# Optimization experiments

Hardware: AMD Instinct MI355X
Metric: run time of the kernel (lower is better)

The kernel has to match this reference:

```python
import jax, jax.numpy as jnp
import numpy as np

D_EMB, N_HEADS = 1024, 16
D_K = D_EMB // N_HEADS

def setup_inputs() -> dict:
    key = jax.random.key(0)
    ks = jax.random.split(key, 5)
    scale = 0.02
    return {
        "n": jax.random.normal(ks[0], (2, 2048, D_EMB), dtype=jnp.float32),
        "W_q": jax.random.normal(ks[1], (D_EMB, D_EMB), dtype=jnp.float32) * scale,
        "W_k": jax.random.normal(ks[2], (D_EMB, D_EMB), dtype=jnp.float32) * scale,
        "W_v": jax.random.normal(ks[3], (D_EMB, D_EMB), dtype=jnp.float32) * scale,
        "W_o": jax.random.normal(ks[4], (D_EMB, D_EMB), dtype=jnp.float32) * scale,
    }

def reference(n, W_q, W_k, W_v, W_o):
    B, S, _ = n.shape
    # torch Linear(bias=False): y = x @ W.T, W is [out, in]
    def proj(x, W):
        y = jnp.einsum('bsd,ed->bse', x, W)
        return y.reshape(B, S, N_HEADS, D_K).transpose(0, 2, 1, 3)  # [B,H,S,Dk]
    Q, K, V = proj(n, W_q), proj(n, W_k), proj(n, W_v)
    A = jnp.einsum('bhqd,bhkd->bhqk', Q, K) * (D_K ** -0.5)
    A = jnp.clip(A, -5.0, 5.0)
    A = jax.nn.softmax(A, axis=-1)
    ctx = jnp.einsum('bhqk,bhkd->bhqd', A, V)  # [B,H,S,Dk]
    ctx = ctx.transpose(0, 2, 1, 3).reshape(B, S, D_EMB)
    return jnp.einsum('bsd,ed->bse', ctx, W_o)
```

## Files before the change

kernel.cpp:

```cpp
#include <hip/hip_runtime.h>
#include <hip/hip_bf16.h>
#include <stdint.h>

typedef __attribute__((ext_vector_type(4))) float floatx4;
typedef __attribute__((ext_vector_type(8))) short shortx8;
typedef __attribute__((ext_vector_type(4))) unsigned short ushortx4;
typedef __attribute__((ext_vector_type(8))) unsigned short ushortx8;
typedef __attribute__((ext_vector_type(2))) uint32_t uintx2;

#define MFMA16(a, b, c) __builtin_amdgcn_mfma_f32_16x16x32_bf16((a), (b), (c), 0, 0, 0)

__device__ inline unsigned short f2bf(float f) {
    union { float f; uint32_t u; } v; v.f = f;
    uint32_t u = v.u;
    return (unsigned short)((u + 0x7FFFu + ((u >> 16) & 1u)) >> 16);
}

#if defined(__has_builtin) && __has_builtin(__builtin_amdgcn_cvt_pk_bf16_f32)
__device__ inline uint32_t pkbf(float a, float b) {
    auto r = __builtin_amdgcn_cvt_pk_bf16_f32(a, b);
    union { decltype(r) v; uint32_t u; } x; x.v = r; return x.u;
}
#else
__device__ inline uint32_t pkbf(float a, float b) {
    return ((uint32_t)f2bf(b) << 16) | f2bf(a);
}
#endif

#if defined(__has_builtin) && __has_builtin(__builtin_amdgcn_exp2f)
#define EXP2F(x) __builtin_amdgcn_exp2f(x)
#else
#define EXP2F(x) __expf((x) * 0.69314718056f)
#endif

__device__ inline void gl2lds16(const void* g, void* l) {
    __builtin_amdgcn_global_load_lds(
        (const __attribute__((address_space(1))) void*)(uintptr_t)g,
        (__attribute__((address_space(3))) void*)(uintptr_t)l, 16, 0, 0);
}

__global__ void convert_all(const float* __restrict__ n, const float* __restrict__ wq,
                            const float* __restrict__ wk, const float* __restrict__ wv,
                            const float* __restrict__ wo,
                            unsigned short* __restrict__ nb, unsigned short* __restrict__ wqb,
                            unsigned short* __restrict__ wkb, unsigned short* __restrict__ wvb,
                            unsigned short* __restrict__ wob) {
    int i = blockIdx.x * 256 + threadIdx.x;
    const float* src; unsigned short* dst; int off;
    if (i < 1048576) { src = n; dst = nb; off = i; }
    else {
        int j = i - 1048576; int r = j >> 18; int o = j & 262143;
        src = (r == 0) ? wq : (r == 1) ? wk : (r == 2) ? wv : wo;
        dst = (r == 0) ? wqb : (r == 1) ? wkb : (r == 2) ? wvb : wob;
        off = o;
    }
    floatx4 f = ((const floatx4*)src)[off];
    uintx2 u;
    u.x = pkbf(f.x, f.y); u.y = pkbf(f.z, f.w);
    ((uintx2*)dst)[off] = u;
}

__device__ inline void gemm_tile_128(const unsigned short* __restrict__ A,
                                     const unsigned short* __restrict__ B,
                                     unsigned short* sA, unsigned short* sB,
                                     floatx4 acc[4][4]) {
    const int tid = threadIdx.x, w = tid >> 6, l = tid & 63;
    const int c = l & 15, quad = l >> 4;
    const int wm = (w >> 1) * 64, wn = (w & 1) * 64;
    for (int kt = 0; kt < 16; ++kt) {
        #pragma unroll
        for (int r = 0; r < 4; ++r) {
            int row = r * 32 + w * 8 + (l >> 3);
            int cb  = (l & 7) ^ (row & 7);
            gl2lds16(A + row * 1024 + kt * 64 + cb * 8, (char*)sA + r * 4096 + w * 1024 + l * 16);
            gl2lds16(B + row * 1024 + kt * 64 + cb * 8, (char*)sB + r * 4096 + w * 1024 + l * 16);
        }
        __syncthreads();
        #pragma unroll
        for (int ks = 0; ks < 2; ++ks) {
            shortx8 af[4], bfr[4];
            #pragma unroll
            for (int i2 = 0; i2 < 4; ++i2) {
                int ra = wm + i2 * 16 + c;
                af[i2] = *(const shortx8*)((const char*)sA + ra * 128 + (((ks * 4 + quad) ^ (ra & 7)) * 16));
                int rb = wn + i2 * 16 + c;
                bfr[i2] = *(const shortx8*)((const char*)sB + rb * 128 + (((ks * 4 + quad) ^ (rb & 7)) * 16));
            }
            #pragma unroll
            for (int i2 = 0; i2 < 4; ++i2)
                #pragma unroll
                for (int j2 = 0; j2 < 4; ++j2)
                    acc[i2][j2] = MFMA16(af[i2], bfr[j2], acc[i2][j2]);
        }
        __syncthreads();
    }
}

__global__ void gemm_qkv(const unsigned short* __restrict__ nb,
                         const unsigned short* __restrict__ wqb,
                         const unsigned short* __restrict__ wkb,
                         const unsigned short* __restrict__ wvb,
                         unsigned short* __restrict__ Qb, unsigned short* __restrict__ Kb,
                         unsigned short* __restrict__ VTg) {
    __shared__ unsigned short sAB[2 * 128 * 64];
    unsigned short* sA = sAB;
    unsigned short* sB = sAB + 128 * 64;
    const int mt = blockIdx.x, nt = blockIdx.y;
    const int region = nt >> 3, nl0 = (nt & 7) * 128;
    const unsigned short* W = (region == 0) ? wqb : (region == 1) ? wkb : wvb;
    floatx4 acc[4][4] = {};
    gemm_tile_128(nb + mt * 128 * 1024, W + nl0 * 1024, sA, sB, acc);
    const int tid = threadIdx.x, w = tid >> 6, l = tid & 63, c = l & 15, quad = l >> 4;
    const int wm = (w >> 1) * 64, wn = (w & 1) * 64;
    if (region < 2) {
        unsigned short* O = (region == 0) ? Qb : Kb;
        #pragma unroll
        for (int i2 = 0; i2 < 4; ++i2)
            #pragma unroll
            for (int j2 = 0; j2 < 4; ++j2)
                #pragma unroll
                for (int r = 0; r < 4; ++r) {
                    int row = wm + i2 * 16 + quad * 4 + r, col = wn + j2 * 16 + c;
                    sAB[row * 128 + col] = f2bf(acc[i2][j2][r]);
                }
        __syncthreads();
        #pragma unroll
        for (int t = 0; t < 8; ++t) {
            int off = t * 4096 + tid * 16;
            int row = off >> 8, colb = off & 255;
            *(ushortx8*)((char*)(O + (mt * 128 + row) * 1024 + nl0) + colb) =
                *(const ushortx8*)((const char*)sAB + off);
        }
    } else {
        const int hh = w & 1, tt = w >> 1;
        char* img = (char*)sAB + (hh * 2 + tt) * 8192;
        #pragma unroll
        for (int i2 = 0; i2 < 4; ++i2)
            #pragma unroll
            for (int j2 = 0; j2 < 4; ++j2) {
                int d = j2 * 16 + c;
                int blk = (i2 >> 1) * 4 + quad;
                int phys = blk ^ (d & 7);
                uintx2 v;
                v.x = pkbf(acc[i2][j2][0], acc[i2][j2][1]);
                v.y = pkbf(acc[i2][j2][2], acc[i2][j2][3]);
                *(uintx2*)(img + d * 128 + phys * 16 + (i2 & 1) * 8) = v;
            }
        __syncthreads();
        const int h0 = (nt & 7) * 2, t0 = mt * 2;
        #pragma unroll
        for (int g = 0; g < 8; ++g) {
            int off = g * 4096 + tid * 16;
            int hsel = off >> 14, within = off & 16383;
            *(ushortx8*)((char*)VTg + (h0 + hsel) * 524288 + t0 * 8192 + within) =
                *(const ushortx8*)((const char*)sAB + off);
        }
    }
}

__global__ void __launch_bounds__(256) gemm_out(const unsigned short* __restrict__ ctx,
                         const unsigned short* __restrict__ wob,
                         float* __restrict__ out) {
    __shared__ unsigned short sA[128 * 64];
    __shared__ unsigned short sB[64 * 64];
    __shared__ float sC[64 * 64];
    const int mt = blockIdx.x, nt = blockIdx.y;
    const unsigned short* A = ctx + mt * 128 * 1024;
    const unsigned short* B = wob + nt * 64 * 1024;
    const int tid = threadIdx.x, w = tid >> 6, l = tid & 63, c = l & 15, quad = l >> 4;
    const int srow = w * 8 + (l >> 3), scb = l & 7;
    floatx4 acc[2][4] = {};
    for (int kt = 0; kt < 16; ++kt) {
        #pragma unroll
        for (int r = 0; r < 4; ++r) {
            int row = r * 32 + srow, cb = scb ^ (row & 7);
            gl2lds16(A + row * 1024 + kt * 64 + cb * 8, (char*)sA + r * 4096 + w * 1024 + l * 16);
        }
        #pragma unroll
        for (int r = 0; r < 2; ++r) {
            int row = r * 32 + srow, cb = scb ^ (row & 7);
            gl2lds16(B + row * 1024 + kt * 64 + cb * 8, (char*)sB + r * 4096 + w * 1024 + l * 16);
        }
        __syncthreads();
        #pragma unroll
        for (int ks = 0; ks < 2; ++ks) {
            shortx8 af[2], bf2[4];
            #pragma unroll
            for (int i2 = 0; i2 < 2; ++i2) {
                int ra = w * 32 + i2 * 16 + c;
                af[i2] = *(const shortx8*)((const char*)sA + ra * 128 + (((ks * 4 + quad) ^ (ra & 7)) * 16));
            }
            #pragma unroll
            for (int j2 = 0; j2 < 4; ++j2) {
                int rb = j2 * 16 + c;
                bf2[j2] = *(const shortx8*)((const char*)sB + rb * 128 + (((ks * 4 + quad) ^ (rb & 7)) * 16));
            }
            #pragma unroll
            for (int i2 = 0; i2 < 2; ++i2)
                #pragma unroll
                for (int j2 = 0; j2 < 4; ++j2)
                    acc[i2][j2] = MFMA16(af[i2], bf2[j2], acc[i2][j2]);
        }
        __syncthreads();
    }
    #pragma unroll
    for (int half = 0; half < 2; ++half) {
        if ((w >> 1) == half) {
            #pragma unroll
            for (int i2 = 0; i2 < 2; ++i2)
                #pragma unroll
                for (int j2 = 0; j2 < 4; ++j2)
                    #pragma unroll
                    for (int r = 0; r < 4; ++r) {
                        int row = (w & 1) * 32 + i2 * 16 + quad * 4 + r, col = j2 * 16 + c;
                        sC[row * 64 + col] = acc[i2][j2][r];
                    }
        }
        __syncthreads();
        #pragma unroll
        for (int t = 0; t < 4; ++t) {
            int off = t * 4096 + tid * 16;
            int row = off >> 8, colb = off & 255;
            *(floatx4*)((char*)(out + (mt * 128 + half * 64 + row) * 1024 + nt * 64) + colb) =
                *(const floatx4*)((const char*)sC + off);
        }
        __syncthreads();
    }
}

__global__ void __launch_bounds__(256) attn(const unsigned short* __restrict__ Qb,
                     const unsigned short* __restrict__ Kb,
                     const unsigned short* __restrict__ VTg, unsigned short* __restrict__ ctx) {
    __shared__ unsigned short sQ[128 * 64];
    __shared__ unsigned short sK[2][64 * 64];
    __shared__ unsigned short sV[2][64 * 64];
    const int qt = blockIdx.x, h = blockIdx.y, b = blockIdx.z;
    const int tid = threadIdx.x, w = tid >> 6, l = tid & 63, c = l & 15, quad = l >> 4;
    const int tok0 = b * 2048 + qt * 128;
    const int srow = w * 8 + (l >> 3), scb = l & 7;
    #pragma unroll
    for (int r = 0; r < 4; ++r) {
        int row = r * 32 + srow, cb = scb ^ (row & 7);
        gl2lds16(Qb + (tok0 + row) * 1024 + h * 64 + cb * 8, (char*)sQ + r * 4096 + w * 1024 + l * 16);
    }
    const unsigned short* Kbase = Kb + b * 2048 * 1024 + h * 64;
    const char* Vbase = (const char*)VTg + h * 524288 + (size_t)b * 32 * 8192;
    #pragma unroll
    for (int r = 0; r < 2; ++r) {
        int row = r * 32 + srow, cb = scb ^ (row & 7);
        gl2lds16(Kbase + row * 1024 + cb * 8, (char*)sK[0] + r * 4096 + w * 1024 + l * 16);
        gl2lds16(Vbase + r * 4096 + w * 1024 + l * 16, (char*)sV[0] + r * 4096 + w * 1024 + l * 16);
    }
    __syncthreads();
    shortx8 qf[2][2];
    #pragma unroll
    for (int ks = 0; ks < 2; ++ks)
        #pragma unroll
        for (int qb = 0; qb < 2; ++qb) {
            int rq = w * 32 + qb * 16 + c;
            qf[ks][qb] = *(const shortx8*)((const char*)sQ + rq * 128 + (((ks * 4 + quad) ^ (rq & 7)) * 16));
        }
    floatx4 cacc[4][2] = {};
    float lacc[2] = {0.f, 0.f};
    const float SC = 0.18033688f;
    const float CLIP = 7.2134752f;
    for (int kt = 0; kt < 32; ++kt) {
        const int cur = kt & 1;
        if (kt < 31) {
            #pragma unroll
            for (int r = 0; r < 2; ++r) {
                int row = r * 32 + srow, cb = scb ^ (row & 7);
                gl2lds16(Kbase + ((kt + 1) * 64 + row) * 1024 + cb * 8,
                         (char*)sK[cur ^ 1] + r * 4096 + w * 1024 + l * 16);
                gl2lds16(Vbase + (kt + 1) * 8192 + r * 4096 + w * 1024 + l * 16,
                         (char*)sV[cur ^ 1] + r * 4096 + w * 1024 + l * 16);
            }
        }
        const unsigned short* sKc = sK[cur];
        const unsigned short* sVc = sV[cur];
        floatx4 s[2][4] = {};
        #pragma unroll
        for (int ks = 0; ks < 2; ++ks) {
            shortx8 ak[4];
            #pragma unroll
            for (int j = 0; j < 4; ++j) {
                int rk = j * 16 + c;
                ak[j] = *(const shortx8*)((const char*)sKc + rk * 128 + (((ks * 4 + quad) ^ (rk & 7)) * 16));
            }
            #pragma unroll
            for (int j = 0; j < 4; ++j)
                #pragma unroll
                for (int qb = 0; qb < 2; ++qb)
                    s[qb][j] = MFMA16(ak[j], qf[ks][qb], s[qb][j]);
        }
        #pragma unroll
        for (int qb = 0; qb < 2; ++qb) {
            float rs = 0.f;
            #pragma unroll
            for (int j = 0; j < 4; ++j)
                #pragma unroll
                for (int r = 0; r < 4; ++r) {
                    float v = s[qb][j][r] * SC;
                    v = fminf(fmaxf(v, -CLIP), CLIP);
                    v = EXP2F(v);
                    s[qb][j][r] = v;
                    rs += v;
                }
            rs += __shfl_xor(rs, 16);
            rs += __shfl_xor(rs, 32);
            lacc[qb] += rs;
        }
        #pragma unroll
        for (int chunk = 0; chunk < 2; ++chunk) {
            shortx8 av[4];
            #pragma unroll
            for (int di = 0; di < 4; ++di) {
                int rv = di * 16 + c;
                av[di] = *(const shortx8*)((const char*)sVc + rv * 128 + (((chunk * 4 + quad) ^ (rv & 7)) * 16));
            }
            shortx8 p[2];
            #pragma unroll
            for (int qb = 0; qb < 2; ++qb) {
                union { shortx8 v; uint32_t u[4]; } pk;
                pk.u[0] = pkbf(s[qb][2 * chunk][0], s[qb][2 * chunk][1]);
                pk.u[1] = pkbf(s[qb][2 * chunk][2], s[qb][2 * chunk][3]);
                pk.u[2] = pkbf(s[qb][2 * chunk + 1][0], s[qb][2 * chunk + 1][1]);
                pk.u[3] = pkbf(s[qb][2 * chunk + 1][2], s[qb][2 * chunk + 1][3]);
                p[qb] = pk.v;
            }
            #pragma unroll
            for (int di = 0; di < 4; ++di)
                #pragma unroll
                for (int qb = 0; qb < 2; ++qb)
                    cacc[di][qb] = MFMA16(av[di], p[qb], cacc[di][qb]);
        }
        if (kt < 31) __syncthreads();
    }
    #pragma unroll
    for (int qb = 0; qb < 2; ++qb) {
        float inv = 1.0f / lacc[qb];
        int row = tok0 + w * 32 + qb * 16 + c;
        #pragma unroll
        for (int di = 0; di < 4; ++di) {
            uintx2 v;
            v.x = pkbf(cacc[di][qb][0] * inv, cacc[di][qb][1] * inv);
            v.y = pkbf(cacc[di][qb][2] * inv, cacc[di][qb][3] * inv);
            *(uintx2*)(ctx + row * 1024 + h * 64 + di * 16 + quad * 4) = v;
        }
    }
}

extern "C" void kernel_launch(void* const* d_in, const int* in_sizes, int n_in,
                              void* d_out, int out_size, void* d_ws, size_t ws_size,
                              hipStream_t stream) {
    const float* n  = (const float*)d_in[0];
    const float* wq = (const float*)d_in[1];
    const float* wk = (const float*)d_in[2];
    const float* wv = (const float*)d_in[3];
    const float* wo = (const float*)d_in[4];
    float* out = (float*)d_out;
    char* ws = (char*)d_ws;
    unsigned short* nb  = (unsigned short*)(ws);
    unsigned short* wqb = (unsigned short*)(ws + 8388608);
    unsigned short* wkb = (unsigned short*)(ws + 10485760);
    unsigned short* wvb = (unsigned short*)(ws + 12582912);
    unsigned short* wob = (unsigned short*)(ws + 14680064);
    unsigned short* Qb  = (unsigned short*)(ws + 16777216);
    unsigned short* Kb  = (unsigned short*)(ws + 25165824);
    unsigned short* VTg = (unsigned short*)(ws + 33554432);
    unsigned short* ctx = (unsigned short*)(ws + 41943040);

    convert_all<<<dim3(8192), dim3(256), 0, stream>>>(n, wq, wk, wv, wo, nb, wqb, wkb, wvb, wob);
    gemm_qkv<<<dim3(32, 24), dim3(256), 0, stream>>>(nb, wqb, wkb, wvb, Qb, Kb, VTg);
    attn<<<dim3(16, 16, 2), dim3(256), 0, stream>>>(Qb, Kb, VTg, ctx);
    gemm_out<<<dim3(32, 16), dim3(256), 0, stream>>>(ctx, wob, out);
}
```

Measured before the change: 190.6 us.

## Process two KV tiles per attention iteration with quad-buffered LDS

```diff
diff --git a/kernel.cpp b/kernel.cpp
--- a/kernel.cpp
+++ b/kernel.cpp
@@ -31,6 +31,12 @@
 #define EXP2F(x) __builtin_amdgcn_exp2f(x)
 #else
 #define EXP2F(x) __expf((x) * 0.69314718056f)
+#endif
+
+#if defined(__has_builtin) && __has_builtin(__builtin_amdgcn_fmed3f)
+#define CLAMP3(x, lo, hi) __builtin_amdgcn_fmed3f((x), (lo), (hi))
+#else
+#define CLAMP3(x, lo, hi) fminf(fmaxf((x), (lo)), (hi))
 #endif
 
 __device__ inline void gl2lds16(const void* g, void* l) {
@@ -228,113 +234,89 @@
     }
 }
 
-__global__ void __launch_bounds__(256) attn(const unsigned short* __restrict__ Qb,
+__global__ void __launch_bounds__(256, 2) attn(const unsigned short* __restrict__ Qb,
                      const unsigned short* __restrict__ Kb,
                      const unsigned short* __restrict__ VTg, unsigned short* __restrict__ ctx) {
-    __shared__ unsigned short sQ[128 * 64];
-    __shared__ unsigned short sK[2][64 * 64];
-    __shared__ unsigned short sV[2][64 * 64];
+    __shared__ char lds[81920];
     const int qt = blockIdx.x, h = blockIdx.y, b = blockIdx.z;
     const int tid = threadIdx.x, w = tid >> 6, l = tid & 63, c = l & 15, quad = l >> 4;
     const int tok0 = b * 2048 + qt * 128;
-    const int srow = w * 8 + (l >> 3), scb = l & 7;
+    const int srow = w * 8 + (l >> 3);
+    const int cb = (l & 7) ^ (srow & 7);
     #pragma unroll
-    for (int r = 0; r < 4; ++r) {
-        int row = r * 32 + srow, cb = scb ^ (row & 7);
-        gl2lds16(Qb + (tok0 + row) * 1024 + h * 64 + cb * 8, (char*)sQ + r * 4096 + w * 1024 + l * 16);
-    }
+    for (int r = 0; r < 4; ++r)
+        gl2lds16(Qb + (tok0 + r * 32 + srow) * 1024 + h * 64 + cb * 8, lds + r * 4096 + w * 1024 + l * 16);
     const unsigned short* Kbase = Kb + b * 2048 * 1024 + h * 64;
-    const char* Vbase = (const char*)VTg + h * 524288 + (size_t)b * 32 * 8192;
-    #pragma unroll
-    for (int r = 0; r < 2; ++r) {
-        int row = r * 32 + srow, cb = scb ^ (row & 7);
-        gl2lds16(Kbase + row * 1024 + cb * 8, (char*)sK[0] + r * 4096 + w * 1024 + l * 16);
-        gl2lds16(Vbase + r * 4096 + w * 1024 + l * 16, (char*)sV[0] + r * 4096 + w * 1024 + l * 16);
-    }
+    const char* Vbase = (const char*)VTg + h * 524288 + (size_t)b * 262144;
+    const char* Ksrc = (const char*)(Kbase + srow * 1024 + cb * 8);
+    #define STAGE_K(kt, t) { _Pragma("unroll") for (int r = 0; r < 2; ++r) \
+        gl2lds16(Ksrc + (size_t)(kt) * 131072 + r * 65536, lds + 16384 + (t) * 8192 + r * 4096 + w * 1024 + l * 16); }
+    #define STAGE_V(kt, t) { _Pragma("unroll") for (int r = 0; r < 2; ++r) \
+        gl2lds16(Vbase + (kt) * 8192 + r * 4096 + w * 1024 + l * 16, lds + 49152 + (t) * 8192 + r * 4096 + w * 1024 + l * 16); }
+    STAGE_K(0, 0) STAGE_V(0, 0) STAGE_K(1, 1) STAGE_V(1, 1)
     __syncthreads();
+    int lb[2];
+    lb[0] = c * 128 + ((quad ^ (c & 7)) * 16);
+    lb[1] = c * 128 + (((4 + quad) ^ (c & 7)) * 16);
     shortx8 qf[2][2];
     #pragma unroll
     for (int ks = 0; ks < 2; ++ks)
         #pragma unroll
-        for (int qb = 0; qb < 2; ++qb) {
-            int rq = w * 32 + qb * 16 + c;
-            qf[ks][qb] = *(const shortx8*)((const char*)sQ + rq * 128 + (((ks * 4 + quad) ^ (rq & 7)) * 16));
-        }
+        for (int qb = 0; qb < 2; ++qb)
+            qf[ks][qb] = *(const shortx8*)(lds + (w * 2 + qb) * 2048 + lb[ks]);
     floatx4 cacc[4][2] = {};
     float lacc[2] = {0.f, 0.f};
     const float SC = 0.18033688f;
     const float CLIP = 7.2134752f;
-    for (int kt = 0; kt < 32; ++kt) {
-        const int cur = kt & 1;
-        if (kt < 31) {
-            #pragma unroll
-            for (int r = 0; r < 2; ++r) {
-                int row = r * 32 + srow, cb = scb ^ (row & 7);
-                gl2lds16(Kbase + ((kt + 1) * 64 + row) * 1024 + cb * 8,
-                         (char*)sK[cur ^ 1] + r * 4096 + w * 1024 + l * 16);
-                gl2lds16(Vbase + (kt + 1) * 8192 + r * 4096 + w * 1024 + l * 16,
-                         (char*)sV[cur ^ 1] + r * 4096 + w * 1024 + l * 16);
-            }
-        }
-        const unsigned short* sKc = sK[cur];
-        const unsigned short* sVc = sV[cur];
-        floatx4 s[2][4] = {};
-        #pragma unroll
-        for (int ks = 0; ks < 2; ++ks) {
-            shortx8 ak[4];
-            #pragma unroll
-            for (int j = 0; j < 4; ++j) {
-                int rk = j * 16 + c;
-                ak[j] = *(const shortx8*)((const char*)sKc + rk * 128 + (((ks * 4 + quad) ^ (rk & 7)) * 16));
-            }
-            #pragma unroll
-            for (int j = 0; j < 4; ++j)
-                #pragma unroll
-                for (int qb = 0; qb < 2; ++qb)
-                    s[qb][j] = MFMA16(ak[j], qf[ks][qb], s[qb][j]);
-        }
-        #pragma unroll
-        for (int qb = 0; qb < 2; ++qb) {
-            float rs = 0.f;
-            #pragma unroll
-            for (int j = 0; j < 4; ++j)
-                #pragma unroll
-                for (int r = 0; r < 4; ++r) {
-                    float v = s[qb][j][r] * SC;
-                    v = fminf(fmaxf(v, -CLIP), CLIP);
-                    v = EXP2F(v);
-                    s[qb][j][r] = v;
-                    rs += v;
-                }
-            rs += __shfl_xor(rs, 16);
-            rs += __shfl_xor(rs, 32);
-            lacc[qb] += rs;
-        }
-        #pragma unroll
-        for (int chunk = 0; chunk < 2; ++chunk) {
-            shortx8 av[4];
-            #pragma unroll
-            for (int di = 0; di < 4; ++di) {
-                int rv = di * 16 + c;
-                av[di] = *(const shortx8*)((const char*)sVc + rv * 128 + (((chunk * 4 + quad) ^ (rv & 7)) * 16));
-            }
-            shortx8 p[2];
-            #pragma unroll
-            for (int qb = 0; qb < 2; ++qb) {
-                union { shortx8 v; uint32_t u[4]; } pk;
-                pk.u[0] = pkbf(s[qb][2 * chunk][0], s[qb][2 * chunk][1]);
-                pk.u[1] = pkbf(s[qb][2 * chunk][2], s[qb][2 * chunk][3]);
-                pk.u[2] = pkbf(s[qb][2 * chunk + 1][0], s[qb][2 * chunk + 1][1]);
-                pk.u[3] = pkbf(s[qb][2 * chunk + 1][2], s[qb][2 * chunk + 1][3]);
-                p[qb] = pk.v;
-            }
-            #pragma unroll
-            for (int di = 0; di < 4; ++di)
-                #pragma unroll
-                for (int qb = 0; qb < 2; ++qb)
-                    cacc[di][qb] = MFMA16(av[di], p[qb], cacc[di][qb]);
-        }
-        if (kt < 31) __syncthreads();
+
+    #define COMPUTE_S(t, s) { _Pragma("unroll") for (int ks = 0; ks < 2; ++ks) { \
+        shortx8 ak[4]; \
+        _Pragma("unroll") for (int j = 0; j < 4; ++j) \
+            ak[j] = *(const shortx8*)(lds + 16384 + (t) * 8192 + j * 2048 + lb[ks]); \
+        _Pragma("unroll") for (int j = 0; j < 4; ++j) \
+            _Pragma("unroll") for (int qb = 0; qb < 2; ++qb) \
+                s[qb][j] = MFMA16(ak[j], qf[ks][qb], s[qb][j]); } }
+
+    #define SOFTMAX_T(s) { _Pragma("unroll") for (int qb = 0; qb < 2; ++qb) { \
+        float rs = 0.f; \
+        _Pragma("unroll") for (int j = 0; j < 4; ++j) \
+            _Pragma("unroll") for (int r = 0; r < 4; ++r) { \
+                float v = EXP2F(CLAMP3(s[qb][j][r] * SC, -CLIP, CLIP)); \
+                s[qb][j][r] = v; rs += v; } \
+        rs += __shfl_xor(rs, 16); rs += __shfl_xor(rs, 32); \
+        lacc[qb] += rs; } }
+
+    #define PV_T(t, s) { _Pragma("unroll") for (int chunk = 0; chunk < 2; ++chunk) { \
+        shortx8 av[4]; \
+        _Pragma("unroll") for (int di = 0; di < 4; ++di) \
+            av[di] = *(const shortx8*)(lds + 49152 + (t) * 8192 + di * 2048 + lb[chunk]); \
+        shortx8 p[2]; \
+        _Pragma("unroll") for (int qb = 0; qb < 2; ++qb) { \
+            union { shortx8 v; uint32_t u[4]; } pk; \
+            pk.u[0] = pkbf(s[qb][2 * chunk][0], s[qb][2 * chunk][1]); \
+            pk.u[1] = pkbf(s[qb][2 * chunk][2], s[qb][2 * chunk][3]); \
+            pk.u[2] = pkbf(s[qb][2 * chunk + 1][0], s[qb][2 * chunk + 1][1]); \
+            pk.u[3] = pkbf(s[qb][2 * chunk + 1][2], s[qb][2 * chunk + 1][3]); \
+            p[qb] = pk.v; } \
+        _Pragma("unroll") for (int di = 0; di < 4; ++di) \
+            _Pragma("unroll") for (int qb = 0; qb < 2; ++qb) \
+                cacc[di][qb] = MFMA16(av[di], p[qb], cacc[di][qb]); } }
+
+    for (int p = 0; p < 16; ++p) {
+        const int bufA = (p & 1) * 2, bufB = bufA + 1;
+        if (p < 15) {
+            const int nA = bufA ^ 2;
+            STAGE_K(2 * p + 2, nA) STAGE_V(2 * p + 2, nA)
+            STAGE_K(2 * p + 3, nA + 1) STAGE_V(2 * p + 3, nA + 1)
+        }
+        floatx4 sA[2][4] = {}, sB[2][4] = {};
+        COMPUTE_S(bufA, sA)
+        COMPUTE_S(bufB, sB)
+        SOFTMAX_T(sA)
+        PV_T(bufA, sA)
+        SOFTMAX_T(sB)
+        PV_T(bufB, sB)
+        if (p < 15) __syncthreads();
     }
     #pragma unroll
     for (int qb = 0; qb < 2; ++qb) {
```

Result: faster. 177.0 us (-7.1%).

## Split attention warps across key halves with LDS reduction, fold Q scale into projection

Applied to the files above, without the earlier changes.

```diff
diff --git a/kernel.cpp b/kernel.cpp
--- a/kernel.cpp
+++ b/kernel.cpp
@@ -31,6 +31,12 @@
 #define EXP2F(x) __builtin_amdgcn_exp2f(x)
 #else
 #define EXP2F(x) __expf((x) * 0.69314718056f)
+#endif
+
+#if defined(__has_builtin) && __has_builtin(__builtin_amdgcn_fmed3f)
+#define CLAMP3(x, lo, hi) __builtin_amdgcn_fmed3f((x), (lo), (hi))
+#else
+#define CLAMP3(x, lo, hi) fminf(fmaxf((x), (lo)), (hi))
 #endif
 
 __device__ inline void gl2lds16(const void* g, void* l) {
@@ -114,6 +120,7 @@
     const int wm = (w >> 1) * 64, wn = (w & 1) * 64;
     if (region < 2) {
         unsigned short* O = (region == 0) ? Qb : Kb;
+        const float sc = (region == 0) ? 0.18033688f : 1.0f;
         #pragma unroll
         for (int i2 = 0; i2 < 4; ++i2)
             #pragma unroll
@@ -121,7 +128,7 @@
                 #pragma unroll
                 for (int r = 0; r < 4; ++r) {
                     int row = wm + i2 * 16 + quad * 4 + r, col = wn + j2 * 16 + c;
-                    sAB[row * 128 + col] = f2bf(acc[i2][j2][r]);
+                    sAB[row * 128 + col] = f2bf(acc[i2][j2][r] * sc);
                 }
         __syncthreads();
         #pragma unroll
@@ -228,83 +235,77 @@
     }
 }
 
-__global__ void __launch_bounds__(256) attn(const unsigned short* __restrict__ Qb,
+__global__ void __launch_bounds__(256, 2) attn(const unsigned short* __restrict__ Qb,
                      const unsigned short* __restrict__ Kb,
                      const unsigned short* __restrict__ VTg, unsigned short* __restrict__ ctx) {
-    __shared__ unsigned short sQ[128 * 64];
-    __shared__ unsigned short sK[2][64 * 64];
-    __shared__ unsigned short sV[2][64 * 64];
+    __shared__ char lds[81920];
     const int qt = blockIdx.x, h = blockIdx.y, b = blockIdx.z;
     const int tid = threadIdx.x, w = tid >> 6, l = tid & 63, c = l & 15, quad = l >> 4;
+    const int qh = w >> 1, kp = w & 1;
     const int tok0 = b * 2048 + qt * 128;
-    const int srow = w * 8 + (l >> 3), scb = l & 7;
+    const int srow = w * 8 + (l >> 3);
+    const int cb = (l & 7) ^ (srow & 7);
     #pragma unroll
-    for (int r = 0; r < 4; ++r) {
-        int row = r * 32 + srow, cb = scb ^ (row & 7);
-        gl2lds16(Qb + (tok0 + row) * 1024 + h * 64 + cb * 8, (char*)sQ + r * 4096 + w * 1024 + l * 16);
-    }
+    for (int r = 0; r < 4; ++r)
+        gl2lds16(Qb + (tok0 + r * 32 + srow) * 1024 + h * 64 + cb * 8, lds + r * 4096 + w * 1024 + l * 16);
     const unsigned short* Kbase = Kb + b * 2048 * 1024 + h * 64;
-    const char* Vbase = (const char*)VTg + h * 524288 + (size_t)b * 32 * 8192;
-    #pragma unroll
-    for (int r = 0; r < 2; ++r) {
-        int row = r * 32 + srow, cb = scb ^ (row & 7);
-        gl2lds16(Kbase + row * 1024 + cb * 8, (char*)sK[0] + r * 4096 + w * 1024 + l * 16);
-        gl2lds16(Vbase + r * 4096 + w * 1024 + l * 16, (char*)sV[0] + r * 4096 + w * 1024 + l * 16);
-    }
+    const char* Vbase = (const char*)VTg + h * 524288 + (size_t)b * 262144;
+    const char* Ksrc = (const char*)(Kbase + srow * 1024 + cb * 8);
+    #define STAGE_K(kt, t) { _Pragma("unroll") for (int r = 0; r < 2; ++r) \
+        gl2lds16(Ksrc + (size_t)(kt) * 131072 + r * 65536, lds + 16384 + (t) * 8192 + r * 4096 + w * 1024 + l * 16); }
+    #define STAGE_V(kt, t) { _Pragma("unroll") for (int r = 0; r < 2; ++r) \
+        gl2lds16(Vbase + (kt) * 8192 + r * 4096 + w * 1024 + l * 16, lds + 49152 + (t) * 8192 + r * 4096 + w * 1024 + l * 16); }
+    STAGE_K(0, 0) STAGE_V(0, 0) STAGE_K(1, 1) STAGE_V(1, 1)
     __syncthreads();
-    shortx8 qf[2][2];
+    int lb[2];
+    lb[0] = c * 128 + ((quad ^ (c & 7)) * 16);
+    lb[1] = c * 128 + (((4 + quad) ^ (c & 7)) * 16);
+    shortx8 qf[2][4];
     #pragma unroll
     for (int ks = 0; ks < 2; ++ks)
         #pragma unroll
-        for (int qb = 0; qb < 2; ++qb) {
-            int rq = w * 32 + qb * 16 + c;
-            qf[ks][qb] = *(const shortx8*)((const char*)sQ + rq * 128 + (((ks * 4 + quad) ^ (rq & 7)) * 16));
-        }
-    floatx4 cacc[4][2] = {};
-    float lacc[2] = {0.f, 0.f};
-    const float SC = 0.18033688f;
+        for (int qb = 0; qb < 4; ++qb)
+            qf[ks][qb] = *(const shortx8*)(lds + qh * 8192 + qb * 2048 + lb[ks]);
+    floatx4 cacc[4][4] = {};
+    float lacc[4] = {0.f, 0.f, 0.f, 0.f};
     const float CLIP = 7.2134752f;
-    for (int kt = 0; kt < 32; ++kt) {
-        const int cur = kt & 1;
-        if (kt < 31) {
-            #pragma unroll
-            for (int r = 0; r < 2; ++r) {
-                int row = r * 32 + srow, cb = scb ^ (row & 7);
-                gl2lds16(Kbase + ((kt + 1) * 64 + row) * 1024 + cb * 8,
-                         (char*)sK[cur ^ 1] + r * 4096 + w * 1024 + l * 16);
-                gl2lds16(Vbase + (kt + 1) * 8192 + r * 4096 + w * 1024 + l * 16,
-                         (char*)sV[cur ^ 1] + r * 4096 + w * 1024 + l * 16);
-            }
-        }
-        const unsigned short* sKc = sK[cur];
-        const unsigned short* sVc = sV[cur];
-        floatx4 s[2][4] = {};
-        #pragma unroll
-        for (int ks = 0; ks < 2; ++ks) {
+    const floatx4 fz = {0.f, 0.f, 0.f, 0.f};
+    for (int p = 0; p < 16; ++p) {
+        if (p < 15) {
+            const int nb_ = ((p + 1) & 1) * 2;
+            STAGE_K(2 * p + 2, nb_) STAGE_V(2 * p + 2, nb_)
+            STAGE_K(2 * p + 3, nb_ + 1) STAGE_V(2 * p + 3, nb_ + 1)
+        }
+        const int tb = (p & 1) * 2 + kp;
+        floatx4 s[4][4];
+        {
             shortx8 ak[4];
             #pragma unroll
-            for (int j = 0; j < 4; ++j) {
-                int rk = j * 16 + c;
-                ak[j] = *(const shortx8*)((const char*)sKc + rk * 128 + (((ks * 4 + quad) ^ (rk & 7)) * 16));
-            }
-            #pragma unroll
-            for (int j = 0; j < 4; ++j)
-                #pragma unroll
-                for (int qb = 0; qb < 2; ++qb)
-                    s[qb][j] = MFMA16(ak[j], qf[ks][qb], s[qb][j]);
-        }
-        #pragma unroll
-        for (int qb = 0; qb < 2; ++qb) {
+            for (int j = 0; j < 4; ++j)
+                ak[j] = *(const shortx8*)(lds + 16384 + tb * 8192 + j * 2048 + lb[0]);
+            #pragma unroll
+            for (int j = 0; j < 4; ++j)
+                #pragma unroll
+                for (int qb = 0; qb < 4; ++qb)
+                    s[qb][j] = MFMA16(ak[j], qf[0][qb], fz);
+            #pragma unroll
+            for (int j = 0; j < 4; ++j)
+                ak[j] = *(const shortx8*)(lds + 16384 + tb * 8192 + j * 2048 + lb[1]);
+            #pragma unroll
+            for (int j = 0; j < 4; ++j)
+                #pragma unroll
+                for (int qb = 0; qb < 4; ++qb)
+                    s[qb][j] = MFMA16(ak[j], qf[1][qb], s[qb][j]);
+        }
+        #pragma unroll
+        for (int qb = 0; qb < 4; ++qb) {
             float rs = 0.f;
             #pragma unroll
             for (int j = 0; j < 4; ++j)
                 #pragma unroll
                 for (int r = 0; r < 4; ++r) {
-                    float v = s[qb][j][r] * SC;
-                    v = fminf(fmaxf(v, -CLIP), CLIP);
-                    v = EXP2F(v);
-                    s[qb][j][r] = v;
-                    rs += v;
+                    float v = EXP2F(CLAMP3(s[qb][j][r], -CLIP, CLIP));
+                    s[qb][j][r] = v; rs += v;
                 }
             rs += __shfl_xor(rs, 16);
             rs += __shfl_xor(rs, 32);
@@ -314,38 +315,58 @@
         for (int chunk = 0; chunk < 2; ++chunk) {
             shortx8 av[4];
             #pragma unroll
-            for (int di = 0; di < 4; ++di) {
-                int rv = di * 16 + c;
-                av[di] = *(const shortx8*)((const char*)sVc + rv * 128 + (((chunk * 4 + quad) ^ (rv & 7)) * 16));
-            }
-            shortx8 p[2];
-            #pragma unroll
-            for (int qb = 0; qb < 2; ++qb) {
+            for (int di = 0; di < 4; ++di)
+                av[di] = *(const shortx8*)(lds + 49152 + tb * 8192 + di * 2048 + lb[chunk]);
+            shortx8 pq[4];
+            #pragma unroll
+            for (int qb = 0; qb < 4; ++qb) {
                 union { shortx8 v; uint32_t u[4]; } pk;
                 pk.u[0] = pkbf(s[qb][2 * chunk][0], s[qb][2 * chunk][1]);
                 pk.u[1] = pkbf(s[qb][2 * chunk][2], s[qb][2 * chunk][3]);
                 pk.u[2] = pkbf(s[qb][2 * chunk + 1][0], s[qb][2 * chunk + 1][1]);
                 pk.u[3] = pkbf(s[qb][2 * chunk + 1][2], s[qb][2 * chunk + 1][3]);
-                p[qb] = pk.v;
+                pq[qb] = pk.v;
             }
             #pragma unroll
             for (int di = 0; di < 4; ++di)
                 #pragma unroll
-                for (int qb = 0; qb < 2; ++qb)
-                    cacc[di][qb] = MFMA16(av[di], p[qb], cacc[di][qb]);
-        }
-        if (kt < 31) __syncthreads();
-    }
-    #pragma unroll
-    for (int qb = 0; qb < 2; ++qb) {
-        float inv = 1.0f / lacc[qb];
-        int row = tok0 + w * 32 + qb * 16 + c;
-        #pragma unroll
-        for (int di = 0; di < 4; ++di) {
-            uintx2 v;
-            v.x = pkbf(cacc[di][qb][0] * inv, cacc[di][qb][1] * inv);
-            v.y = pkbf(cacc[di][qb][2] * inv, cacc[di][qb][3] * inv);
-            *(uintx2*)(ctx + row * 1024 + h * 64 + di * 16 + quad * 4) = v;
+                for (int qb = 0; qb < 4; ++qb)
+                    cacc[di][qb] = MFMA16(av[di], pq[qb], cacc[di][qb]);
+        }
+        if (p < 15) __syncthreads();
+    }
+    __syncthreads();
+    const int rbase = 16384 + qh * 20480;
+    if (kp) {
+        #pragma unroll
+        for (int di = 0; di < 4; ++di)
+            #pragma unroll
+            for (int qb = 0; qb < 4; ++qb)
+                #pragma unroll
+                for (int r = 0; r < 4; ++r)
+                    *(float*)(lds + rbase + (di * 16 + qb * 4 + r) * 256 + l * 4) = cacc[di][qb][r];
+        #pragma unroll
+        for (int qb = 0; qb < 4; ++qb)
+            *(float*)(lds + rbase + (64 + qb) * 256 + l * 4) = lacc[qb];
+    }
+    __syncthreads();
+    if (!kp) {
+        #pragma unroll
+        for (int qb = 0; qb < 4; ++qb) {
+            float lsum = lacc[qb] + *(const float*)(lds + rbase + (64 + qb) * 256 + l * 4);
+            float inv = 1.0f / lsum;
+            int row = tok0 + qh * 64 + qb * 16 + c;
+            #pragma unroll
+            for (int di = 0; di < 4; ++di) {
+                float o0 = cacc[di][qb][0] + *(const float*)(lds + rbase + (di * 16 + qb * 4 + 0) * 256 + l * 4);
+                float o1 = cacc[di][qb][1] + *(const float*)(lds + rbase + (di * 16 + qb * 4 + 1) * 256 + l * 4);
+                float o2 = cacc[di][qb][2] + *(const float*)(lds + rbase + (di * 16 + qb * 4 + 2) * 256 + l * 4);
+                float o3 = cacc[di][qb][3] + *(const float*)(lds + rbase + (di * 16 + qb * 4 + 3) * 256 + l * 4);
+                uintx2 v;
+                v.x = pkbf(o0 * inv, o1 * inv);
+                v.y = pkbf(o2 * inv, o3 * inv);
+                *(uintx2*)(ctx + row * 1024 + h * 64 + di * 16 + quad * 4) = v;
+            }
         }
     }
 }
```

After: 173.2 us. -9.1%, faster.
